# Kernel optimization log

Measured on AMD Instinct MI355X. Metric: run time of the kernel, lower is better.

Reference implementation:

```python
import jax, jax.numpy as jnp
import numpy as np

D = 128      # embedding dim
T = 8        # message passing rounds (config.training.T)
NV = 4000    # n_vars
NL = 2 * NV  # n_literals
NC = 16000   # n_clauses


def setup_inputs() -> dict:
    key = jax.random.key(0)
    ks = jax.random.split(key, 12)
    s = np.float32(1.0 / np.sqrt(D))
    return {
        "L_state": jax.random.normal(ks[0], (1, NL, D), jnp.float32),
        "C_state": jax.random.normal(ks[1], (1, NC, D), jnp.float32),
        "hidden_L": jnp.zeros((1, NL, D), jnp.float32),
        "hidden_C": jnp.zeros((1, NC, D), jnp.float32),
        # 0/1 literal-clause incidence, ~40 clauses per literal
        "M": (jax.random.uniform(ks[2], (NL, NC)) < 0.0025).astype(jnp.float32),
        "n_vars": NV,
        "W_lc": jax.random.normal(ks[3], (D, D), jnp.float32) * s,
        "b_lc": jnp.zeros((D,), jnp.float32),
        "W_cl": jax.random.normal(ks[4], (D, D), jnp.float32) * s,
        "b_cl": jnp.zeros((D,), jnp.float32),
        "Wih_C": jax.random.normal(ks[5], (4 * D, D), jnp.float32) * s,
        "Whh_C": jax.random.normal(ks[6], (4 * D, D), jnp.float32) * s,
        "bih_C": jnp.zeros((4 * D,), jnp.float32),
        "bhh_C": jnp.zeros((4 * D,), jnp.float32),
        "Wih_L": jax.random.normal(ks[7], (4 * D, 2 * D), jnp.float32) * s,
        "Whh_L": jax.random.normal(ks[8], (4 * D, D), jnp.float32) * s,
        "bih_L": jnp.zeros((4 * D,), jnp.float32),
        "bhh_L": jnp.zeros((4 * D,), jnp.float32),
    }


def lstm_cell(x, h, c, Wih, Whh, bih, bhh):
    # torch nn.LSTM gate order: i, f, g, o
    gates = x @ Wih.T + bih + h @ Whh.T + bhh
    i, f, g, o = jnp.split(gates, 4, axis=-1)
    c_new = jax.nn.sigmoid(f) * c + jax.nn.sigmoid(i) * jnp.tanh(g)
    h_new = jax.nn.sigmoid(o) * jnp.tanh(c_new)
    return h_new, c_new


def reference(L_state, C_state, hidden_L, hidden_C, M, n_vars,
              W_lc, b_lc, W_cl, b_cl,
              Wih_C, Whh_C, bih_C, bhh_C,
              Wih_L, Whh_L, bih_L, bhh_L):
    # Replicates torch flip() as written: slices dim 0 (size 1), so this is
    # effectively identity for n_vars >= 1 (first slice is empty, second is x).
    def flip(x):
        return jnp.concatenate([x[n_vars:2 * n_vars], x[0:n_vars]], axis=0)

    def step(carry, _):
        L, hL, hC = carry
        LC_pre = L @ W_lc.T + b_lc                        # (1, NL, D)
        LC_msgs = jnp.einsum('lc,sld->scd', M, LC_pre)    # M^T @ pre: (1, NC, D)
        Cs, hC = lstm_cell(LC_msgs, hC, hC, Wih_C, Whh_C, bih_C, bhh_C)
        CL_pre = Cs @ W_cl.T + b_cl                       # (1, NC, D)
        CL_msgs = jnp.einsum('lc,scd->sld', M, CL_pre)    # M @ pre: (1, NL, D)
        inp = jnp.concatenate([CL_msgs, flip(L)], axis=2) # (1, NL, 2D)
        L, hL = lstm_cell(inp, hL, hL, Wih_L, Whh_L, bih_L, bhh_L)
        return (L, hL, hC), None

    (L_final, _, _), _ = jax.lax.scan(step, (L_state, hidden_L, hidden_C), None, length=T)
    return L_final
```

## Files before the change

kernel.cpp:

```cpp
#include <hip/hip_runtime.h>

#define DD   128
#define NL   8000
#define NC   16000
#define TSTEPS 8
#define NBF  2
#define ROWW 96
#define COLW 64

#define OS   33
#define SPLITS8 (32 * OS)
#define SPLIT   (SPLITS8 * 8)
#define LSTR 17
#define LSPL (48 * LSTR * 8)
#define L2S  33
#define L2SPL (48 * L2S * 8)

typedef __attribute__((ext_vector_type(8))) short  short8;
typedef __attribute__((ext_vector_type(8))) _Float16 half8;
typedef __attribute__((ext_vector_type(4))) float  f32x4;

__device__ __forceinline__ float frcp(float x) { return __builtin_amdgcn_rcpf(x); }
__device__ __forceinline__ float sigm(float x) { return frcp(1.f + __expf(-x)); }
__device__ __forceinline__ float tanh_(float x) {
  float e = __expf(2.f * x);
  return 1.f - 2.f * frcp(e + 1.f);
}
__device__ __forceinline__ void add4(float4& a, const float4 b) {
  a.x += b.x; a.y += b.y; a.z += b.z; a.w += b.w;
}
__device__ __forceinline__ unsigned short bfround(float v) {
  unsigned u = __float_as_uint(v);
  return (unsigned short)((u + 0x7FFF + ((u >> 16) & 1)) >> 16);
}
__device__ __forceinline__ float bf2f(unsigned short b) {
  return __uint_as_float(((unsigned)b) << 16);
}
__device__ __forceinline__ void splitf16(float v, unsigned short& h, unsigned short& l) {
  _Float16 hh = (_Float16)v;
  float r = v - (float)hh;
  _Float16 ll = (_Float16)r;
  h = __builtin_bit_cast(unsigned short, hh);
  l = __builtin_bit_cast(unsigned short, ll);
}
__device__ __forceinline__ int4 packi4(const unsigned short* p) {
  return make_int4(p[0] | ((int)p[1] << 16), p[2] | ((int)p[3] << 16),
                   p[4] | ((int)p[5] << 16), p[6] | ((int)p[7] << 16));
}

__device__ __forceinline__ void store_oct3(unsigned short* A, int oct, int m,
                                           float4 a, float4 b) {
  float f[8] = {a.x, a.y, a.z, a.w, b.x, b.y, b.z, b.w};
  unsigned short h[8], md[8], lo[8];
  #pragma unroll
  for (int j = 0; j < 8; ++j) {
    h[j] = bfround(f[j]);
    float r1 = f[j] - bf2f(h[j]);
    md[j] = bfround(r1);
    float r2 = r1 - bf2f(md[j]);
    lo[j] = bfround(r2);
  }
  int base = (oct * OS + m) * 8;
  *(int4*)(A + base)             = packi4(h);
  *(int4*)(A + SPLIT + base)     = packi4(md);
  *(int4*)(A + 2 * SPLIT + base) = packi4(lo);
}

__device__ __forceinline__ void store_oct2g(unsigned short* A, int strideS8, int plane,
                                            int oct, int m, float4 a, float4 b) {
  float f[8] = {a.x, a.y, a.z, a.w, b.x, b.y, b.z, b.w};
  unsigned short h[8], lo[8];
  #pragma unroll
  for (int j = 0; j < 8; ++j) splitf16(f[j], h[j], lo[j]);
  int base = (oct * strideS8 + m) * 8;
  *(int4*)(A + base)         = packi4(h);
  *(int4*)(A + plane + base) = packi4(lo);
}

__device__ __forceinline__ void store_half3L(unsigned short* A, int oct, int half, int m,
                                             float4 a) {
  float f[4] = {a.x, a.y, a.z, a.w};
  unsigned short h[4], md[4], lo[4];
  #pragma unroll
  for (int j = 0; j < 4; ++j) {
    h[j] = bfround(f[j]);
    float r1 = f[j] - bf2f(h[j]);
    md[j] = bfround(r1);
    float r2 = r1 - bf2f(md[j]);
    lo[j] = bfround(r2);
  }
  int base = (oct * LSTR + m) * 8 + half * 4;
  *(int2*)(A + base)            = make_int2(h[0]  | ((int)h[1]  << 16), h[2]  | ((int)h[3]  << 16));
  *(int2*)(A + LSPL + base)     = make_int2(md[0] | ((int)md[1] << 16), md[2] | ((int)md[3] << 16));
  *(int2*)(A + 2 * LSPL + base) = make_int2(lo[0] | ((int)lo[1] << 16), lo[2] | ((int)lo[3] << 16));
}

#define MFMA6(ACC, AH, AM, AL, BH, BM, BL)                                   \
  ACC = __builtin_amdgcn_mfma_f32_16x16x32_bf16(AH, BH, ACC, 0, 0, 0);       \
  ACC = __builtin_amdgcn_mfma_f32_16x16x32_bf16(AH, BM, ACC, 0, 0, 0);       \
  ACC = __builtin_amdgcn_mfma_f32_16x16x32_bf16(AM, BH, ACC, 0, 0, 0);       \
  ACC = __builtin_amdgcn_mfma_f32_16x16x32_bf16(AH, BL, ACC, 0, 0, 0);       \
  ACC = __builtin_amdgcn_mfma_f32_16x16x32_bf16(AL, BH, ACC, 0, 0, 0);       \
  ACC = __builtin_amdgcn_mfma_f32_16x16x32_bf16(AM, BM, ACC, 0, 0, 0);

#define MFMA4(ACC, AH, AL, BH, BL)                                           \
  ACC = __builtin_amdgcn_mfma_f32_16x16x32_f16(AH, BH, ACC, 0, 0, 0);        \
  ACC = __builtin_amdgcn_mfma_f32_16x16x32_f16(AH, BL, ACC, 0, 0, 0);        \
  ACC = __builtin_amdgcn_mfma_f32_16x16x32_f16(AL, BH, ACC, 0, 0, 0);        \
  ACC = __builtin_amdgcn_mfma_f32_16x16x32_f16(AL, BL, ACC, 0, 0, 0);


__global__ __launch_bounds__(256) void init_states(
    float4* __restrict__ Lbuf, const float4* __restrict__ L0,
    float4* __restrict__ hL, const float4* __restrict__ hL0,
    float4* __restrict__ hC, const float4* __restrict__ hC0) {
  int i = blockIdx.x * 256 + threadIdx.x, stride = gridDim.x * 256;
  for (int j = i; j < NL * DD / 4; j += stride) { Lbuf[j] = L0[j]; hL[j] = hL0[j]; }
  for (int j = i; j < NC * DD / 4; j += stride) hC[j] = hC0[j];
}

__global__ __launch_bounds__(256) void scan_M(const float4* __restrict__ M4,
                                              int* __restrict__ csr, int* __restrict__ csc,
                                              int* __restrict__ rcnt, int* __restrict__ ccnt) {
  const int total = (NL * NC) / 4;
  int stride = gridDim.x * blockDim.x;
  for (int i = blockIdx.x * blockDim.x + threadIdx.x; i < total; i += stride) {
    float4 v = M4[i];
    if (v.x == 0.f && v.y == 0.f && v.z == 0.f && v.w == 0.f) continue;
    int base = i * 4;
    int l = base / NC;
    int c0 = base - l * NC;
    float vv[4] = {v.x, v.y, v.z, v.w};
    #pragma unroll
    for (int e = 0; e < 4; ++e) {
      if (vv[e] != 0.f) {
        int c = c0 + e;
        int rp = atomicAdd(&rcnt[l], 1);
        if (rp < ROWW) csr[l * ROWW + rp] = c;
        int cp = atomicAdd(&ccnt[c], 1);
        if (cp < COLW) csc[c * COLW + cp] = l;
      }
    }
  }
}

__device__ __forceinline__ void split_store_bf3(float w, int idx, unsigned short* hi,
                                                unsigned short* md, unsigned short* lo) {
  unsigned short h = bfround(w);
  float r1 = w - bf2f(h);
  unsigned short m = bfround(r1);
  float r2 = r1 - bf2f(m);
  hi[idx] = h; md[idx] = m; lo[idx] = bfround(r2);
}

__global__ __launch_bounds__(256) void build_packC(
    const float* __restrict__ WihC, const float* __restrict__ Wlc, const float* __restrict__ WhhC,
    unsigned short* __restrict__ pkhi, unsigned short* __restrict__ pkmd, unsigned short* __restrict__ pklo,
    unsigned short* __restrict__ qkhi, unsigned short* __restrict__ qklo) {
  int i = blockIdx.x * 256 + threadIdx.x;
  int k = i >> 9, n = i & 511;
  float w;
  if (k < 128) {
    float s = 0.f;
    for (int d = 0; d < 128; ++d) s += WihC[n * 128 + d] * Wlc[d * 128 + k];
    w = s;
  } else {
    w = WhhC[n * 128 + (k - 128)];
  }
  int idx = ((k >> 3) * 512 + n) * 8 + (k & 7);
  split_store_bf3(w, idx, pkhi, pkmd, pklo);
  splitf16(w, qkhi[idx], qklo[idx]);
}

__global__ __launch_bounds__(256) void build_packL(
    const float* __restrict__ WihL, const float* __restrict__ Wcl, const float* __restrict__ WhhL,
    unsigned short* __restrict__ pkhi, unsigned short* __restrict__ pkmd, unsigned short* __restrict__ pklo,
    unsigned short* __restrict__ qkhi, unsigned short* __restrict__ qklo) {
  int i = blockIdx.x * 256 + threadIdx.x;
  int k = i >> 9, n = i & 511;
  float w;
  if (k < 128) {
    float s = 0.f;
    for (int d = 0; d < 128; ++d) s += WihL[n * 256 + d] * Wcl[d * 128 + k];
    w = s;
  } else if (k < 256) {
    w = WihL[n * 256 + k];
  } else {
    w = WhhL[n * 128 + (k - 256)];
  }
  int idx = ((k >> 3) * 512 + n) * 8 + (k & 7);
  split_store_bf3(w, idx, pkhi, pkmd, pklo);
  splitf16(w, qkhi[idx], qklo[idx]);
}

__global__ __launch_bounds__(256) void build_bias(
    const float* __restrict__ bihC, const float* __restrict__ bhhC,
    const float* __restrict__ WihC, const float* __restrict__ blc,
    const float* __restrict__ bihL, const float* __restrict__ bhhL,
    const float* __restrict__ WihL, const float* __restrict__ bcl,
    float* __restrict__ bsumC, float* __restrict__ bvecC,
    float* __restrict__ bsumL, float* __restrict__ bvecL) {
  int i = blockIdx.x * 256 + threadIdx.x;
  if (i < 512) {
    bsumC[i] = bihC[i] + bhhC[i];
    float s = 0.f;
    for (int d = 0; d < 128; ++d) s += WihC[i * 128 + d] * blc[d];
    bvecC[i] = s;
  } else if (i < 1024) {
    int n = i - 512;
    bsumL[n] = bihL[n] + bhhL[n];
    float s = 0.f;
    for (int d = 0; d < 128; ++d) s += WihL[n * 256 + d] * bcl[d];
    bvecL[n] = s;
  }
}

__device__ __forceinline__ void clause_epilogue(
    const f32x4 acc[2][4], const float* bsum, const float* bvec, const int* ccnt,
    float* hC, float* Cs, int rowBase, int quad, int cw) {
  float bs_[4], bv_[4];
  #pragma unroll
  for (int g = 0; g < 4; ++g) { bs_[g] = bsum[g * 128 + cw]; bv_[g] = bvec[g * 128 + cw]; }
  #pragma unroll
  for (int mt = 0; mt < 2; ++mt) {
    #pragma unroll
    for (int reg = 0; reg < 4; ++reg) {
      int row = rowBase + mt * 16 + quad * 4 + reg;
      float deg = (float)ccnt[row];
      float co = hC[(size_t)row * DD + cw];
      float iv = acc[mt][0][reg] + bs_[0] + deg * bv_[0];
      float fv = acc[mt][1][reg] + bs_[1] + deg * bv_[1];
      float gv = acc[mt][2][reg] + bs_[2] + deg * bv_[2];
      float ov = acc[mt][3][reg] + bs_[3] + deg * bv_[3];
      float cn = sigm(fv) * co + sigm(iv) * tanh_(gv);
      hC[(size_t)row * DD + cw] = cn;
      Cs[(size_t)row * DD + cw] = sigm(ov) * tanh_(cn);
    }
  }
}

__device__ __forceinline__ void literal_epilogue2(
    const f32x4 acc[2][4], const float* bsum, const float* bvec, const int* rcnt,
    float* hL, float* Lbuf, int rowBase, int quad, int cw) {
  float bs_[4], bv_[4];
  #pragma unroll
  for (int g = 0; g < 4; ++g) { bs_[g] = bsum[g * 128 + cw]; bv_[g] = bvec[g * 128 + cw]; }
  #pragma unroll
  for (int mt = 0; mt < 2; ++mt) {
    #pragma unroll
    for (int reg = 0; reg < 4; ++reg) {
      int row = rowBase + mt * 16 + quad * 4 + reg;
      float deg = (float)rcnt[row];
      float co = hL[(size_t)row * DD + cw];
      float iv = acc[mt][0][reg] + bs_[0] + deg * bv_[0];
      float fv = acc[mt][1][reg] + bs_[1] + deg * bv_[1];
      float gv = acc[mt][2][reg] + bs_[2] + deg * bv_[2];
      float ov = acc[mt][3][reg] + bs_[3] + deg * bv_[3];
      float cn = sigm(fv) * co + sigm(iv) * tanh_(gv);
      hL[(size_t)row * DD + cw] = cn;
      Lbuf[(size_t)row * DD + cw] = sigm(ov) * tanh_(cn);
    }
  }
}


template <int NOCT, bool STAGE_H>
__global__ __launch_bounds__(512, 2) void clause_bf3(
    const float* __restrict__ Lbuf, const int* __restrict__ csc, const int* __restrict__ ccnt,
    const unsigned short* __restrict__ pkhi, const unsigned short* __restrict__ pkmd,
    const unsigned short* __restrict__ pklo,
    const float* __restrict__ bsum, const float* __restrict__ bvec,
    float* __restrict__ hC, float* __restrict__ Cs) {
  __shared__ unsigned short A[3 * SPLIT];
  __shared__ int IDX[32 * COLW];
  const int t = threadIdx.x;
  const int rowBase = blockIdx.x * 32;

  ((int4*)IDX)[t] = ((const int4*)(csc + rowBase * COLW))[t];
  __syncthreads();

  {
    const int r = t >> 4, sub = t & 15;
    const int c = rowBase + r;
    int cnt = ccnt[c]; if (cnt > COLW) cnt = COLW;
    const int* lst = IDX + r * COLW;
    float4 a0 = make_float4(0, 0, 0, 0), a1 = a0;
    int j = 0;
    for (; j + 8 <= cnt; j += 8) {
      float4 p0[8], p1[8];
      #pragma unroll
      for (int u = 0; u < 8; ++u) {
        const float4* s4 = (const float4*)(Lbuf + (size_t)lst[j + u] * DD) + sub * 2;
        p0[u] = s4[0]; p1[u] = s4[1];
      }
      #pragma unroll
      for (int u = 0; u < 8; ++u) { add4(a0, p0[u]); add4(a1, p1[u]); }
    }
    for (; j < cnt; ++j) {
      const float4* s4 = (const float4*)(Lbuf + (size_t)lst[j] * DD) + sub * 2;
      add4(a0, s4[0]); add4(a1, s4[1]);
    }
    store_oct3(A, sub, r, a0, a1);
    if constexpr (STAGE_H) {
      const float4* h4 = (const float4*)(hC + (size_t)c * DD) + sub * 2;
      store_oct3(A, 16 + sub, r, h4[0], h4[1]);
    }
  }
  __syncthreads();

  const int w = t >> 6, l = t & 63;
  const int quad = l >> 4, lane16 = l & 15;
  const int cw = w * 16 + lane16;
  f32x4 acc[2][4];
  #pragma unroll
  for (int mt = 0; mt < 2; ++mt)
    #pragma unroll
    for (int g = 0; g < 4; ++g) acc[mt][g] = (f32x4){0.f, 0.f, 0.f, 0.f};

  const short8* As = (const short8*)A;
  const short8* Bh = (const short8*)pkhi;
  const short8* Bm = (const short8*)pkmd;
  const short8* Bl = (const short8*)pklo;

  #pragma unroll
  for (int s = 0; s < NOCT / 4; ++s) {
    int ao = (s * 4 + quad) * OS + lane16;
    short8 a0h = As[ao],                a1h = As[ao + 16];
    short8 a0m = As[SPLITS8 + ao],      a1m = As[SPLITS8 + ao + 16];
    short8 a0l = As[2 * SPLITS8 + ao],  a1l = As[2 * SPLITS8 + ao + 16];
    int bo = (s * 4 + quad) * 512 + cw;
    #pragma unroll
    for (int g = 0; g < 4; ++g) {
      short8 bh = Bh[bo + g * 128];
      short8 bm = Bm[bo + g * 128];
      short8 bl = Bl[bo + g * 128];
      MFMA6(acc[0][g], a0h, a0m, a0l, bh, bm, bl);
      MFMA6(acc[1][g], a1h, a1m, a1l, bh, bm, bl);
    }
  }
  clause_epilogue(acc, bsum, bvec, ccnt, hC, Cs, rowBase, quad, cw);
}

template <int NOCT, bool STAGE_H>
__global__ __launch_bounds__(512, 2) void literal_bf3(
    const float* __restrict__ Cs, const int* __restrict__ csr, const int* __restrict__ rcnt,
    const unsigned short* __restrict__ pkhi, const unsigned short* __restrict__ pkmd,
    const unsigned short* __restrict__ pklo,
    const float* __restrict__ bsum, const float* __restrict__ bvec,
    float* __restrict__ hL, float* __restrict__ Lbuf) {
  __shared__ unsigned short A[3 * LSPL];
  __shared__ int IDX[16 * ROWW];
  const int t = threadIdx.x;
  const int rowBase = blockIdx.x * 16;

  if (t < 384) ((int4*)IDX)[t] = ((const int4*)(csr + rowBase * ROWW))[t];
  __syncthreads();

  {
    const int r = t >> 5, cg2 = t & 31;
    const int lr = rowBase + r;
    int cnt = rcnt[lr]; if (cnt > ROWW) cnt = ROWW;
    const int* lst = IDX + r * ROWW;
    float4 a0 = make_float4(0, 0, 0, 0);
    int j = 0;
    for (; j + 8 <= cnt; j += 8) {
      float4 p[8];
      #pragma unroll
      for (int u = 0; u < 8; ++u)
        p[u] = ((const float4*)(Cs + (size_t)lst[j + u] * DD))[cg2];
      #pragma unroll
      for (int u = 0; u < 8; ++u) add4(a0, p[u]);
    }
    for (; j < cnt; ++j)
      add4(a0, ((const float4*)(Cs + (size_t)lst[j] * DD))[cg2]);
    store_half3L(A, cg2 >> 1, cg2 & 1, r, a0);
    store_half3L(A, 16 + (cg2 >> 1), cg2 & 1, r,
                 ((const float4*)(Lbuf + (size_t)lr * DD))[cg2]);
    if constexpr (STAGE_H)
      store_half3L(A, 32 + (cg2 >> 1), cg2 & 1, r,
                   ((const float4*)(hL + (size_t)lr * DD))[cg2]);
  }
  __syncthreads();

  const int w = t >> 6, l = t & 63;
  const int quad = l >> 4, lane16 = l & 15;
  const int cw = w * 16 + lane16;
  f32x4 acc[4];
  #pragma unroll
  for (int g = 0; g < 4; ++g) acc[g] = (f32x4){0.f, 0.f, 0.f, 0.f};

  const short8* As = (const short8*)A;
  const short8* Bh = (const short8*)pkhi;
  const short8* Bm = (const short8*)pkmd;
  const short8* Bl = (const short8*)pklo;

  #pragma unroll
  for (int s = 0; s < NOCT / 4; ++s) {
    int ao = (s * 4 + quad) * LSTR + lane16;
    short8 ah = As[ao];
    short8 am = As[LSPL / 8 + ao];
    short8 al = As[2 * (LSPL / 8) + ao];
    int bo = (s * 4 + quad) * 512 + cw;
    #pragma unroll
    for (int g = 0; g < 4; ++g) {
      short8 bh = Bh[bo + g * 128];
      short8 bm = Bm[bo + g * 128];
      short8 bl = Bl[bo + g * 128];
      MFMA6(acc[g], ah, am, al, bh, bm, bl);
    }
  }

  float bs_[4], bv_[4];
  #pragma unroll
  for (int g = 0; g < 4; ++g) { bs_[g] = bsum[g * 128 + cw]; bv_[g] = bvec[g * 128 + cw]; }
  #pragma unroll
  for (int reg = 0; reg < 4; ++reg) {
    int row = rowBase + quad * 4 + reg;
    float deg = (float)rcnt[row];
    float co = hL[(size_t)row * DD + cw];
    float iv = acc[0][reg] + bs_[0] + deg * bv_[0];
    float fv = acc[1][reg] + bs_[1] + deg * bv_[1];
    float gv = acc[2][reg] + bs_[2] + deg * bv_[2];
    float ov = acc[3][reg] + bs_[3] + deg * bv_[3];
    float cn = sigm(fv) * co + sigm(iv) * tanh_(gv);
    hL[(size_t)row * DD + cw] = cn;
    Lbuf[(size_t)row * DD + cw] = sigm(ov) * tanh_(cn);
  }
}


__global__ __launch_bounds__(512, 2) void clause_f2(
    const float* __restrict__ Lbuf, const int* __restrict__ csc, const int* __restrict__ ccnt,
    const unsigned short* __restrict__ qkhi, const unsigned short* __restrict__ qklo,
    const float* __restrict__ bsum, const float* __restrict__ bvec,
    float* __restrict__ hC, float* __restrict__ Cs) {
  __shared__ unsigned short A[2 * SPLIT];
  __shared__ int IDX[32 * COLW];
  const int t = threadIdx.x;
  const int rowBase = blockIdx.x * 32;

  ((int4*)IDX)[t] = ((const int4*)(csc + rowBase * COLW))[t];
  __syncthreads();

  {
    const int r = t >> 4, sub = t & 15;
    const int c = rowBase + r;
    int cnt = ccnt[c]; if (cnt > COLW) cnt = COLW;
    const int* lst = IDX + r * COLW;
    float4 a0 = make_float4(0, 0, 0, 0), a1 = a0;
    int j = 0;
    for (; j + 8 <= cnt; j += 8) {
      float4 p0[8], p1[8];
      #pragma unroll
      for (int u = 0; u < 8; ++u) {
        const float4* s4 = (const float4*)(Lbuf + (size_t)lst[j + u] * DD) + sub * 2;
        p0[u] = s4[0]; p1[u] = s4[1];
      }
      #pragma unroll
      for (int u = 0; u < 8; ++u) { add4(a0, p0[u]); add4(a1, p1[u]); }
    }
    for (; j < cnt; ++j) {
      const float4* s4 = (const float4*)(Lbuf + (size_t)lst[j] * DD) + sub * 2;
      add4(a0, s4[0]); add4(a1, s4[1]);
    }
    store_oct2g(A, OS, SPLIT, sub, r, a0, a1);
    const float4* h4 = (const float4*)(hC + (size_t)c * DD) + sub * 2;
    store_oct2g(A, OS, SPLIT, 16 + sub, r, h4[0], h4[1]);
  }
  __syncthreads();

  const int w = t >> 6, l = t & 63;
  const int quad = l >> 4, lane16 = l & 15;
  const int cw = w * 16 + lane16;
  f32x4 acc[2][4];
  #pragma unroll
  for (int mt = 0; mt < 2; ++mt)
    #pragma unroll
    for (int g = 0; g < 4; ++g) acc[mt][g] = (f32x4){0.f, 0.f, 0.f, 0.f};

  const half8* As = (const half8*)A;
  const half8* Bh = (const half8*)qkhi;
  const half8* Bl = (const half8*)qklo;

  #pragma unroll
  for (int s = 0; s < 8; ++s) {
    int ao = (s * 4 + quad) * OS + lane16;
    half8 a0h = As[ao],           a1h = As[ao + 16];
    half8 a0l = As[SPLITS8 + ao], a1l = As[SPLITS8 + ao + 16];
    int bo = (s * 4 + quad) * 512 + cw;
    #pragma unroll
    for (int g = 0; g < 4; ++g) {
      half8 bh = Bh[bo + g * 128];
      half8 bl = Bl[bo + g * 128];
      MFMA4(acc[0][g], a0h, a0l, bh, bl);
      MFMA4(acc[1][g], a1h, a1l, bh, bl);
    }
  }
  clause_epilogue(acc, bsum, bvec, ccnt, hC, Cs, rowBase, quad, cw);
}

__global__ __launch_bounds__(512, 2) void literal_f2(
    const float* __restrict__ Cs, const int* __restrict__ csr, const int* __restrict__ rcnt,
    const unsigned short* __restrict__ qkhi, const unsigned short* __restrict__ qklo,
    const float* __restrict__ bsum, const float* __restrict__ bvec,
    float* __restrict__ hL, float* __restrict__ Lbuf) {
  __shared__ unsigned short A[2 * L2SPL];
  __shared__ int IDX[32 * ROWW];
  const int t = threadIdx.x;
  const int rowBase = blockIdx.x * 32;

  ((int4*)IDX)[t] = ((const int4*)(csr + rowBase * ROWW))[t];
  if (t < 256) ((int4*)IDX)[t + 512] = ((const int4*)(csr + rowBase * ROWW))[t + 512];
  __syncthreads();

  {
    const int r = t >> 4, sub = t & 15;
    const int lr = rowBase + r;
    int cnt = rcnt[lr]; if (cnt > ROWW) cnt = ROWW;
    const int* lst = IDX + r * ROWW;
    float4 a0 = make_float4(0, 0, 0, 0), a1 = a0;
    int j = 0;
    for (; j + 8 <= cnt; j += 8) {
      float4 p0[8], p1[8];
      #pragma unroll
      for (int u = 0; u < 8; ++u) {
        const float4* s4 = (const float4*)(Cs + (size_t)lst[j + u] * DD) + sub * 2;
        p0[u] = s4[0]; p1[u] = s4[1];
      }
      #pragma unroll
      for (int u = 0; u < 8; ++u) { add4(a0, p0[u]); add4(a1, p1[u]); }
    }
    for (; j < cnt; ++j) {
      const float4* s4 = (const float4*)(Cs + (size_t)lst[j] * DD) + sub * 2;
      add4(a0, s4[0]); add4(a1, s4[1]);
    }
    store_oct2g(A, L2S, L2SPL, sub, r, a0, a1);
    const float4* l4 = (const float4*)(Lbuf + (size_t)lr * DD) + sub * 2;
    store_oct2g(A, L2S, L2SPL, 16 + sub, r, l4[0], l4[1]);
    const float4* h4 = (const float4*)(hL + (size_t)lr * DD) + sub * 2;
    store_oct2g(A, L2S, L2SPL, 32 + sub, r, h4[0], h4[1]);
  }
  __syncthreads();

  const int w = t >> 6, l = t & 63;
  const int quad = l >> 4, lane16 = l & 15;
  const int cw = w * 16 + lane16;
  f32x4 acc[2][4];
  #pragma unroll
  for (int mt = 0; mt < 2; ++mt)
    #pragma unroll
    for (int g = 0; g < 4; ++g) acc[mt][g] = (f32x4){0.f, 0.f, 0.f, 0.f};

  const half8* As = (const half8*)A;
  const half8* Bh = (const half8*)qkhi;
  const half8* Bl = (const half8*)qklo;

  #pragma unroll
  for (int s = 0; s < 12; ++s) {
    int ao = (s * 4 + quad) * L2S + lane16;
    half8 a0h = As[ao],             a1h = As[ao + 16];
    half8 a0l = As[L2SPL / 8 + ao], a1l = As[L2SPL / 8 + ao + 16];
    int bo = (s * 4 + quad) * 512 + cw;
    #pragma unroll
    for (int g = 0; g < 4; ++g) {
      half8 bh = Bh[bo + g * 128];
      half8 bl = Bl[bo + g * 128];
      MFMA4(acc[0][g], a0h, a0l, bh, bl);
      MFMA4(acc[1][g], a1h, a1l, bh, bl);
    }
  }
  literal_epilogue2(acc, bsum, bvec, rcnt, hL, Lbuf, rowBase, quad, cw);
}


extern "C" void kernel_launch(void* const* d_in, const int* in_sizes, int n_in,
                              void* d_out, int out_size, void* d_ws, size_t ws_size,
                              hipStream_t stream) {
  const float* L0   = (const float*)d_in[0];
  const float* hL0  = (const float*)d_in[2];
  const float* hC0  = (const float*)d_in[3];
  const float* M    = (const float*)d_in[4];
  const float* Wlc  = (const float*)d_in[6];
  const float* blc  = (const float*)d_in[7];
  const float* Wcl  = (const float*)d_in[8];
  const float* bcl  = (const float*)d_in[9];
  const float* WihC = (const float*)d_in[10];
  const float* WhhC = (const float*)d_in[11];
  const float* bihC = (const float*)d_in[12];
  const float* bhhC = (const float*)d_in[13];
  const float* WihL = (const float*)d_in[14];
  const float* WhhL = (const float*)d_in[15];
  const float* bihL = (const float*)d_in[16];
  const float* bhhL = (const float*)d_in[17];

  float* ws    = (float*)d_ws;
  float* hL    = ws;
  float* hC    = hL + NL * DD;
  float* Cs    = hC + NC * DD;
  float* bsumC = Cs + NC * DD;
  float* bvecC = bsumC + 512;
  float* bsumL = bvecC + 512;
  float* bvecL = bsumL + 512;
  unsigned short* pkChi = (unsigned short*)(bvecL + 512);
  unsigned short* pkCmd = pkChi + 256 * 512;
  unsigned short* pkClo = pkCmd + 256 * 512;
  unsigned short* pkLhi = pkClo + 256 * 512;
  unsigned short* pkLmd = pkLhi + 384 * 512;
  unsigned short* pkLlo = pkLmd + 384 * 512;
  unsigned short* qkChi = pkLlo + 384 * 512;
  unsigned short* qkClo = qkChi + 256 * 512;
  unsigned short* qkLhi = qkClo + 256 * 512;
  unsigned short* qkLlo = qkLhi + 384 * 512;
  int* csr  = (int*)(qkLlo + 384 * 512);
  int* csc  = csr + NL * ROWW;
  int* rcnt = csc + NC * COLW;
  int* ccnt = rcnt + NL;
  float* Lbuf = (float*)d_out;

  hipMemsetAsync(rcnt, 0, (NL + NC) * sizeof(int), stream);

  init_states<<<1024, 256, 0, stream>>>((float4*)Lbuf, (const float4*)L0,
                                        (float4*)hL, (const float4*)hL0,
                                        (float4*)hC, (const float4*)hC0);

  scan_M<<<4096, 256, 0, stream>>>((const float4*)M, csr, csc, rcnt, ccnt);

  build_packC<<<(256 * 512) / 256, 256, 0, stream>>>(WihC, Wlc, WhhC,
                                                     pkChi, pkCmd, pkClo, qkChi, qkClo);
  build_packL<<<(384 * 512) / 256, 256, 0, stream>>>(WihL, Wcl, WhhL,
                                                     pkLhi, pkLmd, pkLlo, qkLhi, qkLlo);
  build_bias<<<4, 256, 0, stream>>>(bihC, bhhC, WihC, blc, bihL, bhhL, WihL, bcl,
                                    bsumC, bvecC, bsumL, bvecL);

  clause_bf3<16, false><<<NC / 32, 512, 0, stream>>>(Lbuf, csc, ccnt, pkChi, pkCmd, pkClo,
                                                     bsumC, bvecC, hC, Cs);
  literal_bf3<32, false><<<NL / 16, 512, 0, stream>>>(Cs, csr, rcnt, pkLhi, pkLmd, pkLlo,
                                                      bsumL, bvecL, hL, Lbuf);
  for (int t = 1; t < NBF; ++t) {
    clause_bf3<32, true><<<NC / 32, 512, 0, stream>>>(Lbuf, csc, ccnt, pkChi, pkCmd, pkClo,
                                                      bsumC, bvecC, hC, Cs);
    literal_bf3<48, true><<<NL / 16, 512, 0, stream>>>(Cs, csr, rcnt, pkLhi, pkLmd, pkLlo,
                                                       bsumL, bvecL, hL, Lbuf);
  }
  for (int t = NBF; t < TSTEPS; ++t) {
    clause_f2<<<NC / 32, 512, 0, stream>>>(Lbuf, csc, ccnt, qkChi, qkClo,
                                           bsumC, bvecC, hC, Cs);
    literal_f2<<<NL / 32, 512, 0, stream>>>(Cs, csr, rcnt, qkLhi, qkLlo,
                                            bsumL, bvecL, hL, Lbuf);
  }
}
```

Measured before the change: 1.286 ms.

## Double row tiles in literal_bf3 and clause_f2 with chunked double-buffered K staging

literal_bf3 now processes 32 rows per block instead of 16, and clause_f2 processes 64 rows instead of 32. Each B fragment loaded from global is therefore reused across more M tiles. The K dimension is staged in 128-wide chunks, in literal_bf3 through two alternating LDS buffers, so the next chunk's conversion overlaps the current MMAs while the shared-memory footprint stays small. The index-list staging in LDS is dropped in favour of direct global reads of the CSR/CSC lists. The larger tiles raise register pressure (acc[4][4] in clause_f2) and halve the number of blocks per launch, which may reduce occupancy or parallelism.

After: 1.344 ms. 1.05x slower.

```diff
diff --git a/kernel.cpp b/kernel.cpp
--- a/kernel.cpp
+++ b/kernel.cpp
@@ -11,10 +11,14 @@
 #define OS   33
 #define SPLITS8 (32 * OS)
 #define SPLIT   (SPLITS8 * 8)
-#define LSTR 17
-#define LSPL (48 * LSTR * 8)
 #define L2S  33
 #define L2SPL (48 * L2S * 8)
+#define C64  65
+#define CCH  (16 * C64)
+#define CCHS (CCH * 8)
+#define LCH  (16 * 33)
+#define LCHS (LCH * 8)
+#define LBUFS (3 * LCHS)
 
 typedef __attribute__((ext_vector_type(8))) short  short8;
 typedef __attribute__((ext_vector_type(8))) _Float16 half8;
@@ -66,33 +70,33 @@
   *(int4*)(A + 2 * SPLIT + base) = packi4(lo);
 }
 
-__device__ __forceinline__ void store_oct2g(unsigned short* A, int strideS8, int plane,
-                                            int oct, int m, float4 a, float4 b) {
+__device__ __forceinline__ void store_oct3L(unsigned short* A, int oct, int m,
+                                            float4 a, float4 b) {
   float f[8] = {a.x, a.y, a.z, a.w, b.x, b.y, b.z, b.w};
-  unsigned short h[8], lo[8];
-  #pragma unroll
-  for (int j = 0; j < 8; ++j) splitf16(f[j], h[j], lo[j]);
-  int base = (oct * strideS8 + m) * 8;
-  *(int4*)(A + base)         = packi4(h);
-  *(int4*)(A + plane + base) = packi4(lo);
-}
-
-__device__ __forceinline__ void store_half3L(unsigned short* A, int oct, int half, int m,
-                                             float4 a) {
-  float f[4] = {a.x, a.y, a.z, a.w};
-  unsigned short h[4], md[4], lo[4];
-  #pragma unroll
-  for (int j = 0; j < 4; ++j) {
+  unsigned short h[8], md[8], lo[8];
+  #pragma unroll
+  for (int j = 0; j < 8; ++j) {
     h[j] = bfround(f[j]);
     float r1 = f[j] - bf2f(h[j]);
     md[j] = bfround(r1);
     float r2 = r1 - bf2f(md[j]);
     lo[j] = bfround(r2);
   }
-  int base = (oct * LSTR + m) * 8 + half * 4;
-  *(int2*)(A + base)            = make_int2(h[0]  | ((int)h[1]  << 16), h[2]  | ((int)h[3]  << 16));
-  *(int2*)(A + LSPL + base)     = make_int2(md[0] | ((int)md[1] << 16), md[2] | ((int)md[3] << 16));
-  *(int2*)(A + 2 * LSPL + base) = make_int2(lo[0] | ((int)lo[1] << 16), lo[2] | ((int)lo[3] << 16));
+  int base = (oct * 33 + m) * 8;
+  *(int4*)(A + base)            = packi4(h);
+  *(int4*)(A + LCHS + base)     = packi4(md);
+  *(int4*)(A + 2 * LCHS + base) = packi4(lo);
+}
+
+__device__ __forceinline__ void store_oct2g(unsigned short* A, int strideS8, int plane,
+                                            int oct, int m, float4 a, float4 b) {
+  float f[8] = {a.x, a.y, a.z, a.w, b.x, b.y, b.z, b.w};
+  unsigned short h[8], lo[8];
+  #pragma unroll
+  for (int j = 0; j < 8; ++j) splitf16(f[j], h[j], lo[j]);
+  int base = (oct * strideS8 + m) * 8;
+  *(int4*)(A + base)         = packi4(h);
+  *(int4*)(A + plane + base) = packi4(lo);
 }
 
 #define MFMA6(ACC, AH, AM, AL, BH, BM, BL)                                   \
@@ -341,140 +345,157 @@
   clause_epilogue(acc, bsum, bvec, ccnt, hC, Cs, rowBase, quad, cw);
 }
 
-template <int NOCT, bool STAGE_H>
+#define LML(CK, BUFOFF)                                                       \
+  { const short8* As_ = (const short8*)(A + (BUFOFF));                        \
+    _Pragma("unroll")                                                         \
+    for (int s = 0; s < 4; ++s) {                                             \
+      int ao = (s * 4 + quad) * 33 + lane16;                                  \
+      short8 a0h = As_[ao],            a1h = As_[ao + 16];                    \
+      short8 a0m = As_[LCH + ao],      a1m = As_[LCH + ao + 16];              \
+      short8 a0l = As_[2 * LCH + ao],  a1l = As_[2 * LCH + ao + 16];          \
+      int bo = ((CK) * 16 + s * 4 + quad) * 512 + cw;                         \
+      _Pragma("unroll")                                                       \
+      for (int g = 0; g < 4; ++g) {                                           \
+        short8 bh = Bh[bo + g * 128];                                         \
+        short8 bm = Bm[bo + g * 128];                                         \
+        short8 bl = Bl[bo + g * 128];                                         \
+        MFMA6(acc[0][g], a0h, a0m, a0l, bh, bm, bl);                          \
+        MFMA6(acc[1][g], a1h, a1m, a1l, bh, bm, bl);                          \
+      }                                                                       \
+    } }
+
+template <int NCHUNK>
 __global__ __launch_bounds__(512, 2) void literal_bf3(
     const float* __restrict__ Cs, const int* __restrict__ csr, const int* __restrict__ rcnt,
     const unsigned short* __restrict__ pkhi, const unsigned short* __restrict__ pkmd,
     const unsigned short* __restrict__ pklo,
     const float* __restrict__ bsum, const float* __restrict__ bvec,
     float* __restrict__ hL, float* __restrict__ Lbuf) {
-  __shared__ unsigned short A[3 * LSPL];
-  __shared__ int IDX[16 * ROWW];
+  __shared__ unsigned short A[2 * LBUFS];
   const int t = threadIdx.x;
-  const int rowBase = blockIdx.x * 16;
-
-  if (t < 384) ((int4*)IDX)[t] = ((const int4*)(csr + rowBase * ROWW))[t];
-  __syncthreads();
+  const int rowBase = blockIdx.x * 32;
+  const int r = t >> 4, sub = t & 15;
+  const int lr = rowBase + r;
 
   {
-    const int r = t >> 5, cg2 = t & 31;
-    const int lr = rowBase + r;
     int cnt = rcnt[lr]; if (cnt > ROWW) cnt = ROWW;
-    const int* lst = IDX + r * ROWW;
-    float4 a0 = make_float4(0, 0, 0, 0);
+    const int* lst = csr + lr * ROWW;
+    float4 a0 = make_float4(0, 0, 0, 0), a1 = a0;
     int j = 0;
     for (; j + 8 <= cnt; j += 8) {
-      float4 p[8];
-      #pragma unroll
-      for (int u = 0; u < 8; ++u)
-        p[u] = ((const float4*)(Cs + (size_t)lst[j + u] * DD))[cg2];
-      #pragma unroll
-      for (int u = 0; u < 8; ++u) add4(a0, p[u]);
-    }
-    for (; j < cnt; ++j)
-      add4(a0, ((const float4*)(Cs + (size_t)lst[j] * DD))[cg2]);
-    store_half3L(A, cg2 >> 1, cg2 & 1, r, a0);
-    store_half3L(A, 16 + (cg2 >> 1), cg2 & 1, r,
-                 ((const float4*)(Lbuf + (size_t)lr * DD))[cg2]);
-    if constexpr (STAGE_H)
-      store_half3L(A, 32 + (cg2 >> 1), cg2 & 1, r,
-                   ((const float4*)(hL + (size_t)lr * DD))[cg2]);
+      float4 p0[8], p1[8];
+      #pragma unroll
+      for (int u = 0; u < 8; ++u) {
+        const float4* s4 = (const float4*)(Cs + (size_t)lst[j + u] * DD) + sub * 2;
+        p0[u] = s4[0]; p1[u] = s4[1];
+      }
+      #pragma unroll
+      for (int u = 0; u < 8; ++u) { add4(a0, p0[u]); add4(a1, p1[u]); }
+    }
+    for (; j < cnt; ++j) {
+      const float4* s4 = (const float4*)(Cs + (size_t)lst[j] * DD) + sub * 2;
+      add4(a0, s4[0]); add4(a1, s4[1]);
+    }
+    store_oct3L(A, sub, r, a0, a1);
   }
   __syncthreads();
 
   const int w = t >> 6, l = t & 63;
   const int quad = l >> 4, lane16 = l & 15;
   const int cw = w * 16 + lane16;
-  f32x4 acc[4];
-  #pragma unroll
-  for (int g = 0; g < 4; ++g) acc[g] = (f32x4){0.f, 0.f, 0.f, 0.f};
-
-  const short8* As = (const short8*)A;
+  f32x4 acc[2][4];
+  #pragma unroll
+  for (int mt = 0; mt < 2; ++mt)
+    #pragma unroll
+    for (int g = 0; g < 4; ++g) acc[mt][g] = (f32x4){0.f, 0.f, 0.f, 0.f};
+
   const short8* Bh = (const short8*)pkhi;
   const short8* Bm = (const short8*)pkmd;
   const short8* Bl = (const short8*)pklo;
 
-  #pragma unroll
-  for (int s = 0; s < NOCT / 4; ++s) {
-    int ao = (s * 4 + quad) * LSTR + lane16;
-    short8 ah = As[ao];
-    short8 am = As[LSPL / 8 + ao];
-    short8 al = As[2 * (LSPL / 8) + ao];
-    int bo = (s * 4 + quad) * 512 + cw;
-    #pragma unroll
-    for (int g = 0; g < 4; ++g) {
-      short8 bh = Bh[bo + g * 128];
-      short8 bm = Bm[bo + g * 128];
-      short8 bl = Bl[bo + g * 128];
-      MFMA6(acc[g], ah, am, al, bh, bm, bl);
-    }
-  }
-
-  float bs_[4], bv_[4];
-  #pragma unroll
-  for (int g = 0; g < 4; ++g) { bs_[g] = bsum[g * 128 + cw]; bv_[g] = bvec[g * 128 + cw]; }
-  #pragma unroll
-  for (int reg = 0; reg < 4; ++reg) {
-    int row = rowBase + quad * 4 + reg;
-    float deg = (float)rcnt[row];
-    float co = hL[(size_t)row * DD + cw];
-    float iv = acc[0][reg] + bs_[0] + deg * bv_[0];
-    float fv = acc[1][reg] + bs_[1] + deg * bv_[1];
-    float gv = acc[2][reg] + bs_[2] + deg * bv_[2];
-    float ov = acc[3][reg] + bs_[3] + deg * bv_[3];
-    float cn = sigm(fv) * co + sigm(iv) * tanh_(gv);
-    hL[(size_t)row * DD + cw] = cn;
-    Lbuf[(size_t)row * DD + cw] = sigm(ov) * tanh_(cn);
-  }
-}
-
+  const float4* l4 = (const float4*)(Lbuf + (size_t)lr * DD) + sub * 2;
+  float4 x0 = l4[0], x1 = l4[1];
+  LML(0, 0);
+  store_oct3L(A + LBUFS, sub, r, x0, x1);
+  __syncthreads();
+
+  if constexpr (NCHUNK == 3) {
+    const float4* h4 = (const float4*)(hL + (size_t)lr * DD) + sub * 2;
+    float4 y0 = h4[0], y1 = h4[1];
+    LML(1, LBUFS);
+    store_oct3L(A, sub, r, y0, y1);
+    __syncthreads();
+    LML(2, 0);
+  } else {
+    LML(1, LBUFS);
+  }
+  literal_epilogue2(acc, bsum, bvec, rcnt, hL, Lbuf, rowBase, quad, cw);
+}
+
+
+#define CML(CK)                                                               \
+  { _Pragma("unroll")                                                         \
+    for (int s = 0; s < 4; ++s) {                                             \
+      int ao = (s * 4 + quad) * C64 + lane16;                                 \
+      half8 ah0 = As[ao],           ah1 = As[ao + 16],                        \
+            ah2 = As[ao + 32],      ah3 = As[ao + 48];                        \
+      half8 al0 = As[CCH + ao],      al1 = As[CCH + ao + 16],                 \
+            al2 = As[CCH + ao + 32], al3 = As[CCH + ao + 48];                 \
+      int bo = ((CK) * 16 + s * 4 + quad) * 512 + cw;                         \
+      _Pragma("unroll")                                                       \
+      for (int g = 0; g < 4; ++g) {                                           \
+        half8 bh = Bh[bo + g * 128];                                          \
+        half8 bl = Bl[bo + g * 128];                                          \
+        MFMA4(acc[0][g], ah0, al0, bh, bl);                                   \
+        MFMA4(acc[1][g], ah1, al1, bh, bl);                                   \
+        MFMA4(acc[2][g], ah2, al2, bh, bl);                                   \
+        MFMA4(acc[3][g], ah3, al3, bh, bl);                                   \
+      }                                                                       \
+    } }
 
 __global__ __launch_bounds__(512, 2) void clause_f2(
     const float* __restrict__ Lbuf, const int* __restrict__ csc, const int* __restrict__ ccnt,
     const unsigned short* __restrict__ qkhi, const unsigned short* __restrict__ qklo,
     const float* __restrict__ bsum, const float* __restrict__ bvec,
     float* __restrict__ hC, float* __restrict__ Cs) {
-  __shared__ unsigned short A[2 * SPLIT];
-  __shared__ int IDX[32 * COLW];
+  __shared__ unsigned short A[2 * CCHS];
   const int t = threadIdx.x;
-  const int rowBase = blockIdx.x * 32;
-
-  ((int4*)IDX)[t] = ((const int4*)(csc + rowBase * COLW))[t];
-  __syncthreads();
+  const int rowBase = blockIdx.x * 64;
+  const int r = t >> 3, sub = t & 7;
+  const int c = rowBase + r;
 
   {
-    const int r = t >> 4, sub = t & 15;
-    const int c = rowBase + r;
     int cnt = ccnt[c]; if (cnt > COLW) cnt = COLW;
-    const int* lst = IDX + r * COLW;
-    float4 a0 = make_float4(0, 0, 0, 0), a1 = a0;
+    const int* lst = csc + c * COLW;
+    float4 a0 = make_float4(0, 0, 0, 0), a1 = a0, a2 = a0, a3 = a0;
     int j = 0;
-    for (; j + 8 <= cnt; j += 8) {
-      float4 p0[8], p1[8];
-      #pragma unroll
-      for (int u = 0; u < 8; ++u) {
-        const float4* s4 = (const float4*)(Lbuf + (size_t)lst[j + u] * DD) + sub * 2;
-        p0[u] = s4[0]; p1[u] = s4[1];
+    for (; j + 4 <= cnt; j += 4) {
+      float4 p[4][4];
+      #pragma unroll
+      for (int u = 0; u < 4; ++u) {
+        const float4* s4 = (const float4*)(Lbuf + (size_t)lst[j + u] * DD) + sub * 4;
+        p[u][0] = s4[0]; p[u][1] = s4[1]; p[u][2] = s4[2]; p[u][3] = s4[3];
       }
       #pragma unroll
-      for (int u = 0; u < 8; ++u) { add4(a0, p0[u]); add4(a1, p1[u]); }
+      for (int u = 0; u < 4; ++u) {
+        add4(a0, p[u][0]); add4(a1, p[u][1]); add4(a2, p[u][2]); add4(a3, p[u][3]);
+      }
     }
     for (; j < cnt; ++j) {
-      const float4* s4 = (const float4*)(Lbuf + (size_t)lst[j] * DD) + sub * 2;
-      add4(a0, s4[0]); add4(a1, s4[1]);
-    }
-    store_oct2g(A, OS, SPLIT, sub, r, a0, a1);
-    const float4* h4 = (const float4*)(hC + (size_t)c * DD) + sub * 2;
-    store_oct2g(A, OS, SPLIT, 16 + sub, r, h4[0], h4[1]);
+      const float4* s4 = (const float4*)(Lbuf + (size_t)lst[j] * DD) + sub * 4;
+      add4(a0, s4[0]); add4(a1, s4[1]); add4(a2, s4[2]); add4(a3, s4[3]);
+    }
+    store_oct2g(A, C64, CCHS, 2 * sub,     r, a0, a1);
+    store_oct2g(A, C64, CCHS, 2 * sub + 1, r, a2, a3);
   }
   __syncthreads();
 
   const int w = t >> 6, l = t & 63;
   const int quad = l >> 4, lane16 = l & 15;
   const int cw = w * 16 + lane16;
-  f32x4 acc[2][4];
-  #pragma unroll
-  for (int mt = 0; mt < 2; ++mt)
+  f32x4 acc[4][4];
+  #pragma unroll
+  for (int mt = 0; mt < 4; ++mt)
     #pragma unroll
     for (int g = 0; g < 4; ++g) acc[mt][g] = (f32x4){0.f, 0.f, 0.f, 0.f};
 
@@ -482,21 +503,36 @@
   const half8* Bh = (const half8*)qkhi;
   const half8* Bl = (const half8*)qklo;
 
-  #pragma unroll
-  for (int s = 0; s < 8; ++s) {
-    int ao = (s * 4 + quad) * OS + lane16;
-    half8 a0h = As[ao],           a1h = As[ao + 16];
-    half8 a0l = As[SPLITS8 + ao], a1l = As[SPLITS8 + ao + 16];
-    int bo = (s * 4 + quad) * 512 + cw;
-    #pragma unroll
-    for (int g = 0; g < 4; ++g) {
-      half8 bh = Bh[bo + g * 128];
-      half8 bl = Bl[bo + g * 128];
-      MFMA4(acc[0][g], a0h, a0l, bh, bl);
-      MFMA4(acc[1][g], a1h, a1l, bh, bl);
-    }
-  }
-  clause_epilogue(acc, bsum, bvec, ccnt, hC, Cs, rowBase, quad, cw);
+  CML(0);
+  __syncthreads();
+  {
+    const float4* h4 = (const float4*)(hC + (size_t)c * DD) + sub * 4;
+    float4 h0 = h4[0], h1 = h4[1], h2 = h4[2], h3 = h4[3];
+    store_oct2g(A, C64, CCHS, 2 * sub,     r, h0, h1);
+    store_oct2g(A, C64, CCHS, 2 * sub + 1, r, h2, h3);
+  }
+  __syncthreads();
+  CML(1);
+
+  float bs_[4], bv_[4];
+  #pragma unroll
+  for (int g = 0; g < 4; ++g) { bs_[g] = bsum[g * 128 + cw]; bv_[g] = bvec[g * 128 + cw]; }
+  #pragma unroll
+  for (int mt = 0; mt < 4; ++mt) {
+    #pragma unroll
+    for (int reg = 0; reg < 4; ++reg) {
+      int row = rowBase + mt * 16 + quad * 4 + reg;
+      float deg = (float)ccnt[row];
+      float co = hC[(size_t)row * DD + cw];
+      float iv = acc[mt][0][reg] + bs_[0] + deg * bv_[0];
+      float fv = acc[mt][1][reg] + bs_[1] + deg * bv_[1];
+      float gv = acc[mt][2][reg] + bs_[2] + deg * bv_[2];
+      float ov = acc[mt][3][reg] + bs_[3] + deg * bv_[3];
+      float cn = sigm(fv) * co + sigm(iv) * tanh_(gv);
+      hC[(size_t)row * DD + cw] = cn;
+      Cs[(size_t)row * DD + cw] = sigm(ov) * tanh_(cn);
+    }
+  }
 }
 
 __global__ __launch_bounds__(512, 2) void literal_f2(
@@ -634,16 +670,16 @@
 
   clause_bf3<16, false><<<NC / 32, 512, 0, stream>>>(Lbuf, csc, ccnt, pkChi, pkCmd, pkClo,
                                                      bsumC, bvecC, hC, Cs);
-  literal_bf3<32, false><<<NL / 16, 512, 0, stream>>>(Cs, csr, rcnt, pkLhi, pkLmd, pkLlo,
-                                                      bsumL, bvecL, hL, Lbuf);
+  literal_bf3<2><<<NL / 32, 512, 0, stream>>>(Cs, csr, rcnt, pkLhi, pkLmd, pkLlo,
+                                              bsumL, bvecL, hL, Lbuf);
   for (int t = 1; t < NBF; ++t) {
     clause_bf3<32, true><<<NC / 32, 512, 0, stream>>>(Lbuf, csc, ccnt, pkChi, pkCmd, pkClo,
                                                       bsumC, bvecC, hC, Cs);
-    literal_bf3<48, true><<<NL / 16, 512, 0, stream>>>(Cs, csr, rcnt, pkLhi, pkLmd, pkLlo,
-                                                       bsumL, bvecL, hL, Lbuf);
+    literal_bf3<3><<<NL / 32, 512, 0, stream>>>(Cs, csr, rcnt, pkLhi, pkLmd, pkLlo,
+                                                bsumL, bvecL, hL, Lbuf);
   }
   for (int t = NBF; t < TSTEPS; ++t) {
-    clause_f2<<<NC / 32, 512, 0, stream>>>(Lbuf, csc, ccnt, qkChi, qkClo,
+    clause_f2<<<NC / 64, 512, 0, stream>>>(Lbuf, csc, ccnt, qkChi, qkClo,
                                            bsumC, bvecC, hC, Cs);
     literal_f2<<<NL / 32, 512, 0, stream>>>(Cs, csr, rcnt, qkLhi, qkLlo,
                                             bsumL, bvecL, hL, Lbuf);
```
